# Kernel optimization log

Hardware: AMD Instinct MI355X
Metric: run time of the kernel (lower is better)

## Reference

```python
import jax, jax.numpy as jnp
import numpy as np

DIM = 512
HEADS = 8
HD = DIM // HEADS
HIDDEN = 4 * DIM
EPS = 1e-5


def layernorm(x, g, b):
    mu = jnp.mean(x, axis=-1, keepdims=True)
    var = jnp.mean(jnp.square(x - mu), axis=-1, keepdims=True)
    return (x - mu) * jax.lax.rsqrt(var + EPS) * g + b


def setup_inputs() -> dict:
    key = jax.random.key(0)
    ks = jax.random.split(key, 10)
    B, P, N, C = 16, 4, 256, DIM
    s = 1.0 / np.sqrt(C)
    sh = 1.0 / np.sqrt(HIDDEN)
    return {
        "x": jax.random.normal(ks[0], (B, P, N, C), jnp.float32),
        "ln1_g": jnp.ones((C,), jnp.float32),
        "ln1_b": jnp.zeros((C,), jnp.float32),
        "w_qkv": jax.random.uniform(ks[1], (3 * C, C), jnp.float32, -s, s),
        "w_proj": jax.random.uniform(ks[2], (C, C), jnp.float32, -s, s),
        "b_proj": jax.random.uniform(ks[3], (C,), jnp.float32, -s, s),
        "ln2_g": jnp.ones((C,), jnp.float32),
        "ln2_b": jnp.zeros((C,), jnp.float32),
        "w1": jax.random.uniform(ks[4], (HIDDEN, C), jnp.float32, -s, s),
        "b1": jax.random.uniform(ks[5], (HIDDEN,), jnp.float32, -s, s),
        "w2": jax.random.uniform(ks[6], (C, HIDDEN), jnp.float32, -sh, sh),
        "b2": jax.random.uniform(ks[7], (C,), jnp.float32, -sh, sh),
    }


def reference(x, ln1_g, ln1_b, w_qkv, w_proj, b_proj, ln2_g, ln2_b, w1, b1, w2, b2):
    B, P, N, C = x.shape
    # --- attention branch (batched over B, P, heads; same math as the unrolled loops) ---
    h = layernorm(x, ln1_g, ln1_b)
    qkv = jnp.einsum('bpnc,dc->bpnd', h, w_qkv)            # [B,P,N,3C]
    qkv = qkv.reshape(B, P, N, 3, HEADS, HD)
    q, k, v = qkv[..., 0, :, :], qkv[..., 1, :, :], qkv[..., 2, :, :]  # [B,P,N,H,hd]
    scale = HD ** -0.5
    attn = jnp.einsum('bpnhd,bpmhd->bphnm', q * scale, k)  # [B,P,H,N,N]
    attn = jax.nn.softmax(attn, axis=-1)
    o = jnp.einsum('bphnm,bpmhd->bpnhd', attn, v).reshape(B, P, N, C)
    o = jnp.einsum('bpnc,dc->bpnd', o, w_proj) + b_proj
    x = x + o
    # --- MLP branch ---
    h = layernorm(x, ln2_g, ln2_b)
    h = jax.nn.gelu(jnp.einsum('bpnc,hc->bpnh', h, w1) + b1, approximate=False)
    h = jnp.einsum('bpnh,ch->bpnc', h, w2) + b2
    return x + h
```

## Files before the change

### kernel.cpp

```cpp
#include <hip/hip_runtime.h>

typedef __attribute__((ext_vector_type(8))) short short8;
typedef __attribute__((ext_vector_type(4))) float f32x4;
typedef __attribute__((ext_vector_type(4))) unsigned short u16x4;
typedef __attribute__((ext_vector_type(2))) unsigned int u32x2;

__device__ __forceinline__ float bf2f(unsigned short u) {
    return __uint_as_float(((unsigned)u) << 16);
}
__device__ __forceinline__ unsigned short f2bf(float f) {
    unsigned u = __float_as_uint(f);
    u += 0x7fffu + ((u >> 16) & 1u);
    return (unsigned short)(u >> 16);
}
__device__ __forceinline__ unsigned pack2(float lo, float hi) {
    return (unsigned)f2bf(lo) | ((unsigned)f2bf(hi) << 16);
}
__device__ __forceinline__ void load_lds16(const void* g, void* l) {
    __builtin_amdgcn_global_load_lds(
        (const __attribute__((address_space(1))) void*)g,
        (__attribute__((address_space(3))) void*)l, 16, 0, 0);
}
__device__ __forceinline__ bool is_bf16(const unsigned* dt) {
    return *dt == 0x3F803F80u;
}
__device__ __forceinline__ float gelu_fast(float t) {
    float q = t * (1.5957691f + 0.07135482f * t * t);
    float e = __expf(-q);
    return __fdividef(t, 1.0f + e);
}

__global__ __launch_bounds__(512) void cast_all(
    const void* s_wqkv, const void* s_wproj, const void* s_w1, const void* s_w2,
    const void* v0, const void* v1, const void* v2, const void* v3,
    const void* v4, const void* v5, const void* v6,
    unsigned short* d_wqkv, unsigned short* d_wproj, unsigned short* d_w1,
    unsigned short* d_w2, unsigned short* par, const unsigned* dt)
{
    bool isbf = is_bf16(dt);
    int b = blockIdx.x, tid = threadIdx.x;
    if (b < 768) {
        const void* src; unsigned short* dst; int off;
        if (b < 192)      { src = s_wqkv;  dst = d_wqkv;  off = b * 4096; }
        else if (b < 256) { src = s_wproj; dst = d_wproj; off = (b - 192) * 4096; }
        else if (b < 512) { src = s_w1;    dst = d_w1;    off = (b - 256) * 4096; }
        else              { src = s_w2;    dst = d_w2;    off = (b - 512) * 4096; }
        int i = off + tid * 8;
        if (isbf) {
            *(short8*)(dst + i) = *(const short8*)((const unsigned short*)src + i);
        } else {
            const float* s = (const float*)src + i;
            short8 o;
            #pragma unroll
            for (int j = 0; j < 8; ++j) o[j] = (short)f2bf(s[j]);
            *(short8*)(dst + i) = o;
        }
    } else {
        const void* srcs[7]  = {v0, v1, v2, v3, v4, v5, v6};
        const int   sizes[7] = {512, 512, 512, 512, 512, 2048, 512};
        const int   offs[7]  = {0, 512, 1024, 1536, 2048, 2560, 4608};
        int j = b - 768;
        const void* s = srcs[j];
        unsigned short* d = par + offs[j];
        for (int i = tid; i < sizes[j]; i += 512)
            d[i] = isbf ? ((const unsigned short*)s)[i] : f2bf(((const float*)s)[i]);
    }
}

__global__ __launch_bounds__(256) void ln_kernel(
    const void* __restrict__ xin, size_t row0,
    const unsigned* __restrict__ dt, int inmode,
    const unsigned short* __restrict__ g, const unsigned short* __restrict__ b,
    unsigned short* __restrict__ y)
{
    int w = threadIdx.x >> 6, lane = threadIdx.x & 63;
    size_t lr = (size_t)blockIdx.x * 4 + w;
    size_t gr = row0 + lr;
    bool isf32 = (inmode == 1) || (inmode == 0 && !is_bf16(dt));
    float v[8];
    if (isf32) {
        const float* xr = (const float*)xin + (gr << 9) + (lane << 3);
        #pragma unroll
        for (int j = 0; j < 8; ++j) v[j] = xr[j];
    } else {
        short8 raw = *(const short8*)((const unsigned short*)xin + (gr << 9) + (lane << 3));
        #pragma unroll
        for (int j = 0; j < 8; ++j) v[j] = bf2f((unsigned short)raw[j]);
    }
    float sum = 0.f, sq = 0.f;
    #pragma unroll
    for (int j = 0; j < 8; ++j) { sum += v[j]; sq += v[j] * v[j]; }
    #pragma unroll
    for (int off = 32; off > 0; off >>= 1) {
        sum += __shfl_xor(sum, off);
        sq  += __shfl_xor(sq, off);
    }
    float mu  = sum * (1.0f / 512.0f);
    float var = sq * (1.0f / 512.0f) - mu * mu;
    float rs  = rsqrtf(var + 1e-5f);
    short8 gr8 = *(const short8*)(g + (lane << 3));
    short8 br8 = *(const short8*)(b + (lane << 3));
    short8 outv;
    #pragma unroll
    for (int j = 0; j < 8; ++j) {
        float o = (v[j] - mu) * rs * bf2f((unsigned short)gr8[j]) + bf2f((unsigned short)br8[j]);
        outv[j] = (short)f2bf(o);
    }
    *(short8*)(y + (lr << 9) + (lane << 3)) = outv;
}

__global__ __launch_bounds__(256) void gemm8(
    const unsigned short* __restrict__ A, const unsigned short* __restrict__ W,
    const unsigned short* __restrict__ bias,
    const void* __restrict__ resid, size_t rrow0,
    void* __restrict__ out, size_t orow0,
    int NBY, int N, int K, int mode, const unsigned* __restrict__ dt)
{
    constexpr int BN = 128;
    __shared__ char lds[32768];

    int tid = threadIdx.x;
    int w = tid >> 6, lane = tid & 63;
    int l15 = lane & 15, g = lane >> 4;

    int L = blockIdx.x;
    int bx, by;
    if ((NBY & 7) == 0) {
        int nby8 = NBY >> 3;
        int xcd = L & 7, i = L >> 3;
        by = xcd * nby8 + (i % nby8);
        bx = i / nby8;
    } else {
        by = L % NBY;
        bx = L / NBY;
    }
    int m0 = by << 7, n0 = bx << 7;
    int wm = (w >> 1) << 6;
    int wn = (w & 1) << 6;

    int srow_t = tid >> 3;
    int u_t = (tid & 7) ^ (srow_t & 7);
    const unsigned short* gA[4];
    const unsigned short* gB[4];
    #pragma unroll
    for (int j = 0; j < 4; ++j) {
        gA[j] = A + (size_t)(m0 + j * 32 + srow_t) * K + u_t * 8;
        gB[j] = W + (size_t)(n0 + j * 32 + srow_t) * K + u_t * 8;
    }
    int lslot = tid * 16;
    int swz = l15 & 7;

    f32x4 acc[4][4];
    #pragma unroll
    for (int i = 0; i < 4; ++i)
        #pragma unroll
        for (int j = 0; j < 4; ++j) acc[i][j] = (f32x4){0.f, 0.f, 0.f, 0.f};

    for (int k = 0; k < K; k += 64) {
        if (k > 0) __syncthreads();
        #pragma unroll
        for (int j = 0; j < 4; ++j) {
            load_lds16(gA[j] + k, &lds[j * 4096 + lslot]);
            load_lds16(gB[j] + k, &lds[16384 + j * 4096 + lslot]);
        }
        __syncthreads();
        const char* bAct = lds;
        const char* bW = bAct + 16384;
        #pragma unroll
        for (int s = 0; s < 2; ++s) {
            int cs = ((s * 4 + g) ^ swz) << 4;
            short8 wf[4], af[4];
            #pragma unroll
            for (int i = 0; i < 4; ++i)
                wf[i] = *(const short8*)(bW + (wn + i * 16 + l15) * 128 + cs);
            #pragma unroll
            for (int j = 0; j < 4; ++j)
                af[j] = *(const short8*)(bAct + (wm + j * 16 + l15) * 128 + cs);
            #pragma unroll
            for (int i = 0; i < 4; ++i)
                #pragma unroll
                for (int j = 0; j < 4; ++j)
                    acc[i][j] = __builtin_amdgcn_mfma_f32_16x16x32_bf16(wf[i], af[j], acc[i][j], 0, 0, 0);
        }
    }
    __syncthreads();

    if (mode == 2) {
        #pragma unroll
        for (int i = 0; i < 4; ++i) {
            u16x4 bb = *(const u16x4*)(bias + n0 + wn + i * 16 + g * 4);
            #pragma unroll
            for (int j = 0; j < 4; ++j)
                #pragma unroll
                for (int r = 0; r < 4; ++r)
                    acc[i][j][r] = gelu_fast(acc[i][j][r] + bf2f(bb[r]));
        }
    }

    char* tb = (char*)lds;
    #pragma unroll
    for (int j = 0; j < 4; ++j) {
        int mloc = wm + j * 16 + l15;
        char* rowp = tb + mloc * (BN * 2);
        int sw = mloc & (BN / 4 - 2);
        #pragma unroll
        for (int i = 0; i < 4; ++i) {
            int cq = (wn + i * 16 + g * 4) >> 2;
            u32x2 pk = {pack2(acc[i][j][0], acc[i][j][1]),
                        pack2(acc[i][j][2], acc[i][j][3])};
            *(u32x2*)(rowp + ((cq ^ sw) << 3)) = pk;
        }
    }
    __syncthreads();

    int rL = tid >> 4;
    int lc = tid & 15;
    bool inbf = is_bf16(dt);
    int colg = n0 + lc * 8;
    float bv[8];
    if (mode == 1 || mode == 3) {
        short8 bb = *(const short8*)(bias + colg);
        #pragma unroll
        for (int t = 0; t < 8; ++t) bv[t] = bf2f((unsigned short)bb[t]);
    }

    #pragma unroll
    for (int ps = 0; ps < 8; ++ps) {
        int row = ps * 16 + rL;
        int rowL = m0 + row;
        int c16 = lc ^ ((row >> 1) & 15);
        short8 vv = *(const short8*)(tb + row * (BN * 2) + (c16 << 4));

        if (mode == 0 || mode == 2) {
            *(short8*)((unsigned short*)out + (size_t)rowL * N + colg) = vv;
        } else if (mode == 1) {
            size_t rbase = (rrow0 + rowL) * (size_t)N + colg;
            float o8[8];
            if (inbf) {
                short8 rr = *(const short8*)((const unsigned short*)resid + rbase);
                #pragma unroll
                for (int t = 0; t < 8; ++t)
                    o8[t] = bf2f((unsigned short)rr[t]) + bf2f((unsigned short)vv[t]) + bv[t];
            } else {
                f32x4 r0 = *(const f32x4*)((const float*)resid + rbase);
                f32x4 r1 = *(const f32x4*)((const float*)resid + rbase + 4);
                #pragma unroll
                for (int t = 0; t < 4; ++t) {
                    o8[t]     = r0[t] + bf2f((unsigned short)vv[t]) + bv[t];
                    o8[t + 4] = r1[t] + bf2f((unsigned short)vv[t + 4]) + bv[t + 4];
                }
            }
            short8 ov;
            #pragma unroll
            for (int t = 0; t < 8; ++t) ov[t] = (short)f2bf(o8[t]);
            *(short8*)((unsigned short*)out + (size_t)rowL * N + colg) = ov;
        } else {
            size_t rbase = (size_t)rowL * N + colg;
            short8 rr = *(const short8*)((const unsigned short*)resid + rbase);
            float o8[8];
            #pragma unroll
            for (int t = 0; t < 8; ++t)
                o8[t] = bf2f((unsigned short)rr[t]) + bf2f((unsigned short)vv[t]) + bv[t];
            size_t obase = (orow0 + rowL) * (size_t)N + colg;
            if (inbf) {
                short8 ov;
                #pragma unroll
                for (int t = 0; t < 8; ++t) ov[t] = (short)f2bf(o8[t]);
                *(short8*)((unsigned short*)out + obase) = ov;
            } else {
                float* ob = (float*)out + obase;
                *(f32x4*)ob       = (f32x4){o8[0], o8[1], o8[2], o8[3]};
                *(f32x4*)(ob + 4) = (f32x4){o8[4], o8[5], o8[6], o8[7]};
            }
        }
    }
}

__global__ __launch_bounds__(256) void attn_mfma(
    const unsigned short* __restrict__ qkv, unsigned short* __restrict__ o)
{
    __shared__ unsigned short Vt[64 * 256];
    __shared__ unsigned short Ps[4][16 * 256];
    int bp = blockIdx.x >> 3, h = blockIdx.x & 7;
    const unsigned short* base = qkv + (size_t)bp * 256 * 1536;
    int qo = h << 6, ko = 512 + (h << 6), vo = 1024 + (h << 6);
    int tid = threadIdx.x, w = tid >> 6, lane = tid & 63;
    int l15 = lane & 15, g = lane >> 4;

    {
        int d = tid & 63;
        for (int s = tid >> 6; s < 256; s += 4) {
            unsigned short v = base[(size_t)s * 1536 + vo + d];
            *(unsigned short*)((char*)Vt + d * 512 + (((s >> 3) ^ (d & 7)) << 4) + ((s & 7) << 1)) = v;
        }
    }
    __syncthreads();

    unsigned short* P = Ps[w];

    for (int pass = 0; pass < 4; ++pass) {
        int q0 = pass * 64 + w * 16;
        short8 qa[2];
        #pragma unroll
        for (int t = 0; t < 2; ++t)
            qa[t] = *(const short8*)(base + (size_t)(q0 + l15) * 1536 + qo + t * 32 + g * 8);
        f32x4 S[16];
        #pragma unroll
        for (int ns = 0; ns < 16; ++ns) {
            f32x4 a = {0.f, 0.f, 0.f, 0.f};
            #pragma unroll
            for (int t = 0; t < 2; ++t) {
                short8 kb = *(const short8*)(base + (size_t)(ns * 16 + l15) * 1536 + ko + t * 32 + g * 8);
                a = __builtin_amdgcn_mfma_f32_16x16x32_bf16(qa[t], kb, a, 0, 0, 0);
            }
            S[ns] = a;
        }
        float mx[4], sums[4], inv[4];
        #pragma unroll
        for (int r = 0; r < 4; ++r) {
            float m = -1e30f;
            #pragma unroll
            for (int ns = 0; ns < 16; ++ns) m = fmaxf(m, S[ns][r]);
            m *= 0.125f;
            #pragma unroll
            for (int off = 1; off < 16; off <<= 1) m = fmaxf(m, __shfl_xor(m, off));
            mx[r] = m;
            sums[r] = 0.f;
        }
        #pragma unroll
        for (int ns = 0; ns < 16; ++ns)
            #pragma unroll
            for (int r = 0; r < 4; ++r) {
                float p = __expf(S[ns][r] * 0.125f - mx[r]);
                sums[r] += p;
                S[ns][r] = p;
            }
        #pragma unroll
        for (int r = 0; r < 4; ++r) {
            float s2 = sums[r];
            #pragma unroll
            for (int off = 1; off < 16; off <<= 1) s2 += __shfl_xor(s2, off);
            inv[r] = 1.0f / s2;
        }
        #pragma unroll
        for (int ns = 0; ns < 16; ++ns)
            #pragma unroll
            for (int r = 0; r < 4; ++r) {
                int mq = g * 4 + r;
                int s = ns * 16 + l15;
                *(unsigned short*)((char*)P + mq * 512 + (((s >> 3) ^ (mq & 7)) << 4) + ((s & 7) << 1))
                    = f2bf(S[ns][r] * inv[r]);
            }
        f32x4 O[4];
        #pragma unroll
        for (int ds = 0; ds < 4; ++ds) O[ds] = (f32x4){0.f, 0.f, 0.f, 0.f};
        #pragma unroll
        for (int ks = 0; ks < 8; ++ks) {
            int c = (ks * 4 + g) ^ (l15 & 7);
            short8 pa = *(const short8*)((const char*)P + l15 * 512 + (c << 4));
            #pragma unroll
            for (int ds = 0; ds < 4; ++ds) {
                short8 vb = *(const short8*)((const char*)Vt + (ds * 16 + l15) * 512 + (c << 4));
                O[ds] = __builtin_amdgcn_mfma_f32_16x16x32_bf16(pa, vb, O[ds], 0, 0, 0);
            }
        }
        #pragma unroll
        for (int ds = 0; ds < 4; ++ds)
            #pragma unroll
            for (int r = 0; r < 4; ++r) {
                int mq = q0 + g * 4 + r;
                int d = ds * 16 + l15;
                o[((size_t)(bp * 256 + mq) << 9) + (h << 6) + d] = f2bf(O[ds][r]);
            }
    }
}

extern "C" void kernel_launch(void* const* d_in, const int* in_sizes, int n_in,
                              void* d_out, int out_size, void* d_ws, size_t ws_size,
                              hipStream_t stream)
{
    const void* x      = d_in[0];
    const void* ln1_g  = d_in[1];
    const void* ln1_b  = d_in[2];
    const void* w_qkv  = d_in[3];
    const void* w_proj = d_in[4];
    const void* b_proj = d_in[5];
    const void* ln2_g  = d_in[6];
    const void* ln2_b  = d_in[7];
    const void* w1     = d_in[8];
    const void* b1     = d_in[9];
    const void* w2     = d_in[10];
    const void* b2     = d_in[11];
    const unsigned* dt = (const unsigned*)ln1_g;

    const int M = 16384;
    char* ws = (char*)d_ws;
    unsigned short* wqkv_b  = (unsigned short*)(ws);
    unsigned short* wproj_b = (unsigned short*)(ws + 1572864);
    unsigned short* w1_b    = (unsigned short*)(ws + 2097152);
    unsigned short* w2_b    = (unsigned short*)(ws + 4194304);
    unsigned short* par     = (unsigned short*)(ws + 6291456);
    const size_t CAST_END = 6308096;

    unsigned short* p_g1    = par + 0;
    unsigned short* p_b1ln  = par + 512;
    unsigned short* p_bproj = par + 1024;
    unsigned short* p_g2    = par + 1536;
    unsigned short* p_b2ln  = par + 2048;
    unsigned short* p_b1    = par + 2560;
    unsigned short* p_b2    = par + 4608;

    int NC = 64;
    const int cand[7] = {1, 2, 4, 8, 16, 32, 64};
    for (int i = 0; i < 7; ++i) {
        size_t need = CAST_END + (size_t)(M / cand[i]) * 10240;
        if (need <= ws_size) { NC = cand[i]; break; }
    }
    const int R = M / NC;

    char* cb = ws + CAST_END;
    unsigned short* h   = (unsigned short*)(cb);
    unsigned short* qkv = (unsigned short*)(cb + (size_t)R * 1024);
    unsigned short* o   = (unsigned short*)(cb + (size_t)R * 4096);
    unsigned short* x2  = (unsigned short*)(cb + (size_t)R * 5120);
    unsigned short* hid = (unsigned short*)(cb + (size_t)R * 6144);
    unsigned short* h2  = h;

    cast_all<<<775, 512, 0, stream>>>(w_qkv, w_proj, w1, w2,
                                      ln1_g, ln1_b, b_proj, ln2_g, ln2_b, b1, b2,
                                      wqkv_b, wproj_b, w1_b, w2_b, par, dt);

    for (int c = 0; c < NC; ++c) {
        const size_t r0 = (size_t)c * R;
        const int NBY = R / 128;

        ln_kernel<<<R / 4, 256, 0, stream>>>(x, r0, dt, 0, p_g1, p_b1ln, h);
        gemm8<<<(1536 / 128) * NBY, 256, 0, stream>>>(
            h, wqkv_b, nullptr, nullptr, 0, qkv, 0, NBY, 1536, 512, 0, dt);
        attn_mfma<<<(R / 256) * 8, 256, 0, stream>>>(qkv, o);
        gemm8<<<(512 / 128) * NBY, 256, 0, stream>>>(
            o, wproj_b, p_bproj, x, r0, x2, 0, NBY, 512, 512, 1, dt);
        ln_kernel<<<R / 4, 256, 0, stream>>>(x2, 0, dt, 2, p_g2, p_b2ln, h2);
        gemm8<<<(2048 / 128) * NBY, 256, 0, stream>>>(
            h2, w1_b, p_b1, nullptr, 0, hid, 0, NBY, 2048, 512, 2, dt);
        gemm8<<<(512 / 128) * NBY, 256, 0, stream>>>(
            hid, w2_b, p_b2, x2, 0, d_out, r0, NBY, 512, 2048, 3, dt);
    }
}
```

Measured before the change: 312.4 us.

## Add 256x128-tile GEMM for QKV and FC1, use hardware bf16 pack convert

Adds a gemm_big kernel that gives each block a 256-row by 128-column output tile and each wave a 128x64 tile. It is used for the QKV projection and the first MLP layer, which raises reuse of the weight tile and halves the number of blocks. Its epilogue is staged through swizzled LDS in two halves so stores are coalesced. Separately, bf16 packing now uses the v_cvt_pk_bf16_f32 instruction in place of software rounding, in layernorm and in the gemm8 epilogues. The larger tile doubles the accumulator registers and needs 48KB of LDS, which may cut occupancy, and it requires R to be divisible by 256.

Result: no change. 312.5 us (+0.0%).

```diff
diff --git a/kernel.cpp b/kernel.cpp
--- a/kernel.cpp
+++ b/kernel.cpp
@@ -4,6 +4,7 @@
 typedef __attribute__((ext_vector_type(4))) float f32x4;
 typedef __attribute__((ext_vector_type(4))) unsigned short u16x4;
 typedef __attribute__((ext_vector_type(2))) unsigned int u32x2;
+typedef __attribute__((ext_vector_type(4))) unsigned int u32x4;
 
 __device__ __forceinline__ float bf2f(unsigned short u) {
     return __uint_as_float(((unsigned)u) << 16);
@@ -13,8 +14,10 @@
     u += 0x7fffu + ((u >> 16) & 1u);
     return (unsigned short)(u >> 16);
 }
-__device__ __forceinline__ unsigned pack2(float lo, float hi) {
-    return (unsigned)f2bf(lo) | ((unsigned)f2bf(hi) << 16);
+__device__ __forceinline__ unsigned pack2(float a, float b) {
+    unsigned r;
+    asm("v_cvt_pk_bf16_f32 %0, %1, %2" : "=v"(r) : "v"(a), "v"(b));
+    return r;
 }
 __device__ __forceinline__ void load_lds16(const void* g, void* l) {
     __builtin_amdgcn_global_load_lds(
@@ -100,24 +103,22 @@
     float rs  = rsqrtf(var + 1e-5f);
     short8 gr8 = *(const short8*)(g + (lane << 3));
     short8 br8 = *(const short8*)(b + (lane << 3));
-    short8 outv;
-    #pragma unroll
-    for (int j = 0; j < 8; ++j) {
-        float o = (v[j] - mu) * rs * bf2f((unsigned short)gr8[j]) + bf2f((unsigned short)br8[j]);
-        outv[j] = (short)f2bf(o);
-    }
-    *(short8*)(y + (lr << 9) + (lane << 3)) = outv;
-}
-
-__global__ __launch_bounds__(256) void gemm8(
+    float o[8];
+    #pragma unroll
+    for (int j = 0; j < 8; ++j)
+        o[j] = (v[j] - mu) * rs * bf2f((unsigned short)gr8[j]) + bf2f((unsigned short)br8[j]);
+    u32x4 ov = {pack2(o[0], o[1]), pack2(o[2], o[3]),
+                pack2(o[4], o[5]), pack2(o[6], o[7])};
+    *(u32x4*)(y + (lr << 9) + (lane << 3)) = ov;
+}
+
+__global__ __launch_bounds__(256, 2) void gemm_big(
     const unsigned short* __restrict__ A, const unsigned short* __restrict__ W,
     const unsigned short* __restrict__ bias,
-    const void* __restrict__ resid, size_t rrow0,
-    void* __restrict__ out, size_t orow0,
-    int NBY, int N, int K, int mode, const unsigned* __restrict__ dt)
+    unsigned short* __restrict__ out,
+    int NBY, int N, int K, int mode)
 {
-    constexpr int BN = 128;
-    __shared__ char lds[32768];
+    __shared__ char lds[49152];
 
     int tid = threadIdx.x;
     int w = tid >> 6, lane = tid & 63;
@@ -134,6 +135,133 @@
         by = L % NBY;
         bx = L / NBY;
     }
+    int m0 = by << 8, n0 = bx << 7;
+    int wm = (w >> 1) << 7;
+    int wn = (w & 1) << 6;
+
+    int srow = tid >> 3;
+    int u = (tid & 7) ^ (srow & 7);
+    const unsigned short* gA[8];
+    const unsigned short* gB[4];
+    #pragma unroll
+    for (int j = 0; j < 8; ++j)
+        gA[j] = A + (size_t)(m0 + j * 32 + srow) * K + u * 8;
+    #pragma unroll
+    for (int j = 0; j < 4; ++j)
+        gB[j] = W + (size_t)(n0 + j * 32 + srow) * K + u * 8;
+    int lslot = tid * 16;
+    int swz = l15 & 7;
+
+    f32x4 acc[4][8];
+    #pragma unroll
+    for (int i = 0; i < 4; ++i)
+        #pragma unroll
+        for (int j = 0; j < 8; ++j) acc[i][j] = (f32x4){0.f, 0.f, 0.f, 0.f};
+
+    for (int k = 0; k < K; k += 64) {
+        if (k > 0) __syncthreads();
+        #pragma unroll
+        for (int j = 0; j < 8; ++j)
+            load_lds16(gA[j] + k, &lds[j * 4096 + lslot]);
+        #pragma unroll
+        for (int j = 0; j < 4; ++j)
+            load_lds16(gB[j] + k, &lds[32768 + j * 4096 + lslot]);
+        __syncthreads();
+        const char* bAct = lds;
+        const char* bW = lds + 32768;
+        #pragma unroll
+        for (int s = 0; s < 2; ++s) {
+            int cs = ((s * 4 + g) ^ swz) << 4;
+            short8 wf[4];
+            #pragma unroll
+            for (int i = 0; i < 4; ++i)
+                wf[i] = *(const short8*)(bW + (wn + i * 16 + l15) * 128 + cs);
+            #pragma unroll
+            for (int jg = 0; jg < 8; jg += 4) {
+                short8 af[4];
+                #pragma unroll
+                for (int j = 0; j < 4; ++j)
+                    af[j] = *(const short8*)(bAct + (wm + (jg + j) * 16 + l15) * 128 + cs);
+                #pragma unroll
+                for (int i = 0; i < 4; ++i)
+                    #pragma unroll
+                    for (int j = 0; j < 4; ++j)
+                        acc[i][jg + j] = __builtin_amdgcn_mfma_f32_16x16x32_bf16(
+                            wf[i], af[j], acc[i][jg + j], 0, 0, 0);
+            }
+        }
+    }
+    __syncthreads();
+
+    if (mode == 2) {
+        #pragma unroll
+        for (int i = 0; i < 4; ++i) {
+            u16x4 bb = *(const u16x4*)(bias + n0 + wn + i * 16 + g * 4);
+            #pragma unroll
+            for (int j = 0; j < 8; ++j)
+                #pragma unroll
+                for (int r = 0; r < 4; ++r)
+                    acc[i][j][r] = gelu_fast(acc[i][j][r] + bf2f(bb[r]));
+        }
+    }
+
+    #pragma unroll
+    for (int hh = 0; hh < 2; ++hh) {
+        if ((w >> 1) == hh) {
+            #pragma unroll
+            for (int j = 0; j < 8; ++j) {
+                int mloc = j * 16 + l15;
+                char* rowp = lds + mloc * 256;
+                int sw = mloc & 30;
+                #pragma unroll
+                for (int i = 0; i < 4; ++i) {
+                    int cq = (wn + i * 16 + g * 4) >> 2;
+                    u32x2 pk = {pack2(acc[i][j][0], acc[i][j][1]),
+                                pack2(acc[i][j][2], acc[i][j][3])};
+                    *(u32x2*)(rowp + ((cq ^ sw) << 3)) = pk;
+                }
+            }
+        }
+        __syncthreads();
+        int rL = tid >> 4, lc = tid & 15;
+        int colg = n0 + lc * 8;
+        #pragma unroll
+        for (int ps = 0; ps < 8; ++ps) {
+            int row = ps * 16 + rL;
+            int rowL = m0 + hh * 128 + row;
+            int c16 = lc ^ ((row >> 1) & 15);
+            short8 vv = *(const short8*)(lds + row * 256 + (c16 << 4));
+            *(short8*)(out + (size_t)rowL * N + colg) = vv;
+        }
+        if (hh == 0) __syncthreads();
+    }
+}
+
+__global__ __launch_bounds__(256) void gemm8(
+    const unsigned short* __restrict__ A, const unsigned short* __restrict__ W,
+    const unsigned short* __restrict__ bias,
+    const void* __restrict__ resid, size_t rrow0,
+    void* __restrict__ out, size_t orow0,
+    int NBY, int N, int K, int mode, const unsigned* __restrict__ dt)
+{
+    constexpr int BN = 128;
+    __shared__ char lds[32768];
+
+    int tid = threadIdx.x;
+    int w = tid >> 6, lane = tid & 63;
+    int l15 = lane & 15, g = lane >> 4;
+
+    int L = blockIdx.x;
+    int bx, by;
+    if ((NBY & 7) == 0) {
+        int nby8 = NBY >> 3;
+        int xcd = L & 7, i = L >> 3;
+        by = xcd * nby8 + (i % nby8);
+        bx = i / nby8;
+    } else {
+        by = L % NBY;
+        bx = L / NBY;
+    }
     int m0 = by << 7, n0 = bx << 7;
     int wm = (w >> 1) << 6;
     int wn = (w & 1) << 6;
@@ -250,10 +378,9 @@
                     o8[t + 4] = r1[t] + bf2f((unsigned short)vv[t + 4]) + bv[t + 4];
                 }
             }
-            short8 ov;
-            #pragma unroll
-            for (int t = 0; t < 8; ++t) ov[t] = (short)f2bf(o8[t]);
-            *(short8*)((unsigned short*)out + (size_t)rowL * N + colg) = ov;
+            u32x4 ov = {pack2(o8[0], o8[1]), pack2(o8[2], o8[3]),
+                        pack2(o8[4], o8[5]), pack2(o8[6], o8[7])};
+            *(u32x4*)((unsigned short*)out + (size_t)rowL * N + colg) = ov;
         } else {
             size_t rbase = (size_t)rowL * N + colg;
             short8 rr = *(const short8*)((const unsigned short*)resid + rbase);
@@ -263,10 +390,9 @@
                 o8[t] = bf2f((unsigned short)rr[t]) + bf2f((unsigned short)vv[t]) + bv[t];
             size_t obase = (orow0 + rowL) * (size_t)N + colg;
             if (inbf) {
-                short8 ov;
-                #pragma unroll
-                for (int t = 0; t < 8; ++t) ov[t] = (short)f2bf(o8[t]);
-                *(short8*)((unsigned short*)out + obase) = ov;
+                u32x4 ov = {pack2(o8[0], o8[1]), pack2(o8[2], o8[3]),
+                            pack2(o8[4], o8[5]), pack2(o8[6], o8[7])};
+                *(u32x4*)((unsigned short*)out + obase) = ov;
             } else {
                 float* ob = (float*)out + obase;
                 *(f32x4*)ob       = (f32x4){o8[0], o8[1], o8[2], o8[3]};
@@ -432,17 +558,18 @@
 
     for (int c = 0; c < NC; ++c) {
         const size_t r0 = (size_t)c * R;
-        const int NBY = R / 128;
+        const int NBY  = R / 128;
+        const int NBY2 = R / 256;
 
         ln_kernel<<<R / 4, 256, 0, stream>>>(x, r0, dt, 0, p_g1, p_b1ln, h);
-        gemm8<<<(1536 / 128) * NBY, 256, 0, stream>>>(
-            h, wqkv_b, nullptr, nullptr, 0, qkv, 0, NBY, 1536, 512, 0, dt);
+        gemm_big<<<(1536 / 128) * NBY2, 256, 0, stream>>>(
+            h, wqkv_b, nullptr, qkv, NBY2, 1536, 512, 0);
         attn_mfma<<<(R / 256) * 8, 256, 0, stream>>>(qkv, o);
         gemm8<<<(512 / 128) * NBY, 256, 0, stream>>>(
             o, wproj_b, p_bproj, x, r0, x2, 0, NBY, 512, 512, 1, dt);
         ln_kernel<<<R / 4, 256, 0, stream>>>(x2, 0, dt, 2, p_g2, p_b2ln, h2);
-        gemm8<<<(2048 / 128) * NBY, 256, 0, stream>>>(
-            h2, w1_b, p_b1, nullptr, 0, hid, 0, NBY, 2048, 512, 2, dt);
+        gemm_big<<<(2048 / 128) * NBY2, 256, 0, stream>>>(
+            h2, w1_b, p_b1, hid, NBY2, 2048, 512, 2);
         gemm8<<<(512 / 128) * NBY, 256, 0, stream>>>(
             hid, w2_b, p_b2, x2, 0, d_out, r0, NBY, 512, 2048, 3, dt);
     }
```
